# Optimization experiments

Hardware: AMD Instinct MI355X
Metric: run time of the kernel (lower is better)

The kernel has to match this reference:

```python
import jax, jax.numpy as jnp
import numpy as np

N = 25000
E = 400000
H = 8
C = 32
NEG_SLOPE = 0.2


def setup_inputs() -> dict:
    key = jax.random.key(0)
    ks = iter(jax.random.split(key, 64))
    d = {}
    d['x'] = jax.random.normal(next(ks), (N, 3), jnp.float32)
    d['edge_index'] = jax.random.randint(next(ks), (2, E), 0, N, dtype=jnp.int64)
    d['edge_attr'] = jax.random.uniform(next(ks), (E, 1), jnp.float32)
    # GATv2 layers: dims (in, concat): (3,T) -> (256,T) -> (256,F), out C=32, H=8
    dims = [(3, True), (H * C, True), (H * C, False)]
    for li, (din, concat) in enumerate(dims):
        d[f'Wl{li}'] = jax.random.normal(next(ks), (din, H * C), jnp.float32) * 0.05
        d[f'bl{li}'] = jnp.zeros((H * C,), jnp.float32)
        d[f'Wr{li}'] = jax.random.normal(next(ks), (din, H * C), jnp.float32) * 0.05
        d[f'br{li}'] = jnp.zeros((H * C,), jnp.float32)
        d[f'We{li}'] = jax.random.normal(next(ks), (1, H * C), jnp.float32) * 0.05
        d[f'att{li}'] = jax.random.normal(next(ks), (H, C), jnp.float32) * 0.05
        d[f'bias{li}'] = jnp.zeros((H * C if concat else C,), jnp.float32)
    # node head: Linear(32,32)-ReLU-Linear(32,2)
    d['nh_W1'] = jax.random.normal(next(ks), (C, C), jnp.float32) * 0.05
    d['nh_b1'] = jnp.zeros((C,), jnp.float32)
    d['nh_W2'] = jax.random.normal(next(ks), (C, 2), jnp.float32) * 0.05
    d['nh_b2'] = jnp.zeros((2,), jnp.float32)
    # edge head
    d['eh_W1'] = jax.random.normal(next(ks), (C, C), jnp.float32) * 0.05
    d['eh_b1'] = jnp.zeros((C,), jnp.float32)
    d['eh_W2'] = jax.random.normal(next(ks), (C, 2), jnp.float32) * 0.05
    d['eh_b2'] = jnp.zeros((2,), jnp.float32)
    return d


def _gatv2(x, src, dst, eattr, Wl, bl, Wr, br, We, att, bias, concat):
    n = x.shape[0]
    xl = (x @ Wl + bl).reshape(n, H, C)
    xr = (x @ Wr + br).reshape(n, H, C)
    em = (eattr @ We).reshape(-1, H, C)
    m = jax.nn.leaky_relu(xl[src] + xr[dst] + em, NEG_SLOPE)  # [Et,H,C]
    logit = jnp.einsum('ehc,hc->eh', m, att)                  # [Et,H]
    lmax = jax.ops.segment_max(logit, dst, num_segments=n)
    a = jnp.exp(logit - lmax[dst])
    alpha = a / jax.ops.segment_sum(a, dst, num_segments=n)[dst]
    out = jax.ops.segment_sum(xl[src] * alpha[..., None], dst, num_segments=n)
    out = out.reshape(n, H * C) if concat else out.mean(axis=1)
    return out + bias


def reference(x, edge_index, edge_attr,
              Wl0, bl0, Wr0, br0, We0, att0, bias0,
              Wl1, bl1, Wr1, br1, We1, att1, bias1,
              Wl2, bl2, Wr2, br2, We2, att2, bias2,
              nh_W1, nh_b1, nh_W2, nh_b2,
              eh_W1, eh_b1, eh_W2, eh_b2):
    src0, dst0 = edge_index[0], edge_index[1]
    n = x.shape[0]
    # add_self_loops with fill_value='mean' for edge_attr (PyG GATv2Conv default)
    deg = jax.ops.segment_sum(jnp.ones((src0.shape[0],), x.dtype), dst0, num_segments=n)
    loop_attr = jax.ops.segment_sum(edge_attr, dst0, num_segments=n) / jnp.maximum(deg, 1.0)[:, None]
    ar = jnp.arange(n, dtype=src0.dtype)
    src = jnp.concatenate([src0, ar])
    dst = jnp.concatenate([dst0, ar])
    eattr = jnp.concatenate([edge_attr, loop_attr], axis=0)

    layers = [
        (Wl0, bl0, Wr0, br0, We0, att0, bias0, True),
        (Wl1, bl1, Wr1, br1, We1, att1, bias1, True),
        (Wl2, bl2, Wr2, br2, We2, att2, bias2, False),
    ]
    h = x
    for (Wl, bl, Wr, br, We, att, bias, concat) in layers:
        h = _gatv2(h, src, dst, eattr, Wl, bl, Wr, br, We, att, bias, concat)
        h = jax.nn.relu(h)  # dropout is identity at eval

    node = jax.nn.log_softmax(jax.nn.relu(h @ nh_W1 + nh_b1) @ nh_W2 + nh_b2, axis=1)
    ef = h[src0] + h[dst0]
    edge = jax.nn.log_softmax(jax.nn.relu(ef @ eh_W1 + eh_b1) @ eh_W2 + eh_b2, axis=1)
    return node, edge
```

## Files before the change

kernel.cpp:

```cpp
#include <hip/hip_runtime.h>
#include <math.h>

#define HCDIM 256
#define HEADS 8
#define CH 32
#define NEG 0.2f
#define LOG2E 1.4426950408889634f

typedef __attribute__((ext_vector_type(8))) short bf16x8;
typedef __attribute__((ext_vector_type(4))) float f32x4;

__device__ __forceinline__ float4 ld4(const float* p){ return *reinterpret_cast<const float4*>(p); }
__device__ __forceinline__ void st4(float* p, float a, float b, float c, float d){
    float4 v; v.x=a; v.y=b; v.z=c; v.w=d; *reinterpret_cast<float4*>(p)=v;
}
__device__ __forceinline__ unsigned short f2bf(float f){
    union { float f; unsigned u; } x; x.f = f;
    unsigned r = x.u + 0x7fff + ((x.u >> 16) & 1);
    return (unsigned short)(r >> 16);
}
__device__ __forceinline__ float bf2f(unsigned short u){
    union { unsigned u; float f; } x; x.u = (unsigned)u << 16; return x.f;
}
__device__ __forceinline__ void unpk8(uint4 u, float* x){
    x[0] = __uint_as_float(u.x << 16); x[1] = __uint_as_float(u.x & 0xffff0000u);
    x[2] = __uint_as_float(u.y << 16); x[3] = __uint_as_float(u.y & 0xffff0000u);
    x[4] = __uint_as_float(u.z << 16); x[5] = __uint_as_float(u.z & 0xffff0000u);
    x[6] = __uint_as_float(u.w << 16); x[7] = __uint_as_float(u.w & 0xffff0000u);
}
__device__ __forceinline__ float dpp_sum4(float p){
    p += __int_as_float(__builtin_amdgcn_mov_dpp(__float_as_int(p), 0xB1, 0xf, 0xf, true));
    p += __int_as_float(__builtin_amdgcn_mov_dpp(__float_as_int(p), 0x4E, 0xf, 0xf, true));
    return p;
}

__global__ void k_count(const int* __restrict__ dst, const float* __restrict__ eattr,
                        unsigned long long* __restrict__ degsum,
                        int* __restrict__ rank, int E){
    int e = blockIdx.x*blockDim.x + threadIdx.x;
    if (e < E){
        int d = dst[e];
        unsigned long long pk = (1ULL << 40) |
            (unsigned long long)__float2uint_rn(eattr[e] * 1048576.0f);
        unsigned long long old = atomicAdd(&degsum[d], pk);
        rank[e] = (int)(old >> 40);
    }
}

__global__ __launch_bounds__(1024) void k_scan1(
        const unsigned long long* __restrict__ degsum,
        int* __restrict__ offs, float* __restrict__ lattr,
        int* __restrict__ partials, int n){
    __shared__ int wsum[16];
    int tid = threadIdx.x;
    int i = blockIdx.x*1024 + tid;
    int lane = tid & 63, wid = tid >> 6;
    int x = 0;
    if (i < n){
        unsigned long long ds = degsum[i];
        x = (int)(ds >> 40);
        float ls = (float)(ds & ((1ULL << 40) - 1)) * (1.0f/1048576.0f);
        lattr[i] = ls / fmaxf((float)x, 1.0f);
    }
    int v = x;
    #pragma unroll
    for (int o = 1; o < 64; o <<= 1){
        int y = __shfl_up(v, o);
        if (lane >= o) v += y;
    }
    if (lane == 63) wsum[wid] = v;
    __syncthreads();
    if (wid == 0 && lane < 16){
        int w = wsum[lane];
        #pragma unroll
        for (int o = 1; o < 16; o <<= 1){
            int y = __shfl_up(w, o);
            if (lane >= o) w += y;
        }
        wsum[lane] = w;
    }
    __syncthreads();
    int incl = v + (wid > 0 ? wsum[wid-1] : 0);
    if (i < n) offs[i+1] = incl;
    if (tid == 1023) partials[blockIdx.x] = incl;
}

__global__ __launch_bounds__(1024) void k_scan3(int* __restrict__ offs,
                                                const int* __restrict__ partials, int n){
    __shared__ int sbase;
    if (threadIdx.x < 64){
        int lane = threadIdx.x;
        int vv = (lane < (int)blockIdx.x) ? partials[lane] : 0;
        #pragma unroll
        for (int o = 1; o < 64; o <<= 1) vv += __shfl_xor(vv, o);
        if (lane == 0) sbase = vv;
    }
    __syncthreads();
    int i = blockIdx.x*1024 + threadIdx.x;
    if (i < n) offs[i+1] += sbase;
    if (i == 0) offs[0] = 0;
}

__global__ void k_scatter(const int* __restrict__ src, const int* __restrict__ dst,
                          const float* __restrict__ eattr, const int* __restrict__ offs,
                          const int* __restrict__ rank, int2* csr, int E){
    int e = blockIdx.x*blockDim.x + threadIdx.x;
    if (e < E){
        int d = dst[e];
        int pos = offs[d] + rank[e];
        int2 pk; pk.x = src[e] << 9; pk.y = __float_as_int(eattr[e]);
        csr[pos] = pk;
    }
}

__global__ __launch_bounds__(256) void k_dualgemm(
        const float* __restrict__ h, int din,
        const float* __restrict__ Wl, const float* __restrict__ bl,
        const float* __restrict__ Wr, const float* __restrict__ br,
        unsigned short* __restrict__ xl, unsigned short* __restrict__ xr, int n)
{
    const int ROWS = 16;
    __shared__ float hs[ROWS * HCDIM];
    int row0 = blockIdx.x * ROWS;
    int j = threadIdx.x;

    for (int idx = threadIdx.x; idx < ROWS*din; idx += 256){
        int r = idx / din, k = idx - r*din;
        int row = row0 + r;
        hs[r*din + k] = (row < n) ? h[(size_t)row*din + k] : 0.f;
    }
    __syncthreads();

    float accl[ROWS], accr[ROWS];
    float blj = bl[j], brj = br[j];
    #pragma unroll
    for (int r = 0; r < ROWS; r++){ accl[r] = blj; accr[r] = brj; }

    for (int k = 0; k < din; k++){
        float wl = Wl[k*HCDIM + j], wr = Wr[k*HCDIM + j];
        #pragma unroll
        for (int r = 0; r < ROWS; r++){
            float hv = hs[r*din + k];
            accl[r] += hv*wl;
            accr[r] += hv*wr;
        }
    }
    #pragma unroll
    for (int r = 0; r < ROWS; r++){
        int row = row0 + r;
        if (row < n){
            xl[(size_t)row*HCDIM + j] = f2bf(accl[r]);
            xr[(size_t)row*HCDIM + j] = f2bf(accr[r]);
        }
    }
}

__global__ __launch_bounds__(256) void k_cvtw2(
        const float* __restrict__ Wl1, const float* __restrict__ Wr1,
        const float* __restrict__ Wl2, const float* __restrict__ Wr2,
        unsigned short* __restrict__ Wt1, unsigned short* __restrict__ Wt2)
{
    int idx = blockIdx.x*256 + threadIdx.x;
    int half = idx >> 17;
    int j = idx & 131071;
    int nout = j >> 8, k = j & 255;
    const float* Wl = half ? Wl2 : Wl1;
    const float* Wr = half ? Wr2 : Wr1;
    float v = (nout < 256) ? Wl[k*HCDIM + nout] : Wr[k*HCDIM + (nout - 256)];
    (half ? Wt2 : Wt1)[j] = f2bf(v);
}

#define BM 128
#define BN 128
#define BK 32
#define LDK 40

__global__ __launch_bounds__(256) void k_mfma_gemm(
        const unsigned short* __restrict__ h,
        const unsigned short* __restrict__ Wt,
        const float* __restrict__ bl, const float* __restrict__ br,
        unsigned short* __restrict__ xl, unsigned short* __restrict__ xr, int n)
{
    __shared__ unsigned short As[BM*LDK];
    __shared__ unsigned short Bs[BN*LDK];
    int tid = threadIdx.x;
    int row0 = blockIdx.x * BM;
    int col0 = blockIdx.y * BN;

    int l = tid & 63, w = tid >> 6;
    int wm = (w >> 1) * 64, wn = (w & 1) * 64;

    f32x4 acc[4][4] = {};

    int srow = tid >> 1;
    int skoff = (tid & 1) * 16;

    for (int kt = 0; kt < 8; ++kt){
        int kb = kt * BK;
        uint4 av0, av1;
        int grow = row0 + srow;
        if (grow < n){
            const uint4* ap = reinterpret_cast<const uint4*>(h + (size_t)grow*HCDIM + kb + skoff);
            av0 = ap[0]; av1 = ap[1];
        } else {
            av0.x=av0.y=av0.z=av0.w=0u; av1 = av0;
        }
        const uint4* bp = reinterpret_cast<const uint4*>(Wt + (size_t)(col0+srow)*HCDIM + kb + skoff);
        uint4 bv0 = bp[0], bv1 = bp[1];

        __syncthreads();

        *reinterpret_cast<uint4*>(&As[srow*LDK + skoff])     = av0;
        *reinterpret_cast<uint4*>(&As[srow*LDK + skoff + 8]) = av1;
        *reinterpret_cast<uint4*>(&Bs[srow*LDK + skoff])     = bv0;
        *reinterpret_cast<uint4*>(&Bs[srow*LDK + skoff + 8]) = bv1;

        __syncthreads();

        bf16x8 af[4], bfr[4];
        #pragma unroll
        for (int m = 0; m < 4; m++)
            af[m] = *reinterpret_cast<const bf16x8*>(&As[(wm + m*16 + (l & 15))*LDK + ((l >> 4)*8)]);
        #pragma unroll
        for (int nn = 0; nn < 4; nn++)
            bfr[nn] = *reinterpret_cast<const bf16x8*>(&Bs[(wn + nn*16 + (l & 15))*LDK + ((l >> 4)*8)]);
        #pragma unroll
        for (int m = 0; m < 4; m++)
            #pragma unroll
            for (int nn = 0; nn < 4; nn++)
                acc[m][nn] = __builtin_amdgcn_mfma_f32_16x16x32_bf16(af[m], bfr[nn], acc[m][nn], 0, 0, 0);
    }

    unsigned short* dstp; const float* biasp; int cbase;
    if (col0 < 256){ dstp = xl; biasp = bl; cbase = col0; }
    else           { dstp = xr; biasp = br; cbase = col0 - 256; }

    #pragma unroll
    for (int nn = 0; nn < 4; nn++){
        int gc = cbase + wn + nn*16 + (l & 15);
        float bb = biasp[gc];
        #pragma unroll
        for (int m = 0; m < 4; m++){
            int r0 = row0 + wm + m*16 + ((l >> 4) * 4);
            #pragma unroll
            for (int v = 0; v < 4; v++){
                int rr = r0 + v;
                if (rr < n) dstp[(size_t)rr*HCDIM + gc] = f2bf(acc[m][nn][v] + bb);
            }
        }
    }
}

__global__ __launch_bounds__(256) void k_gat(
        const unsigned short* __restrict__ xl, const unsigned short* __restrict__ xr,
        const int2* __restrict__ csr,
        const int* __restrict__ offs, const float* __restrict__ lattr,
        const float* __restrict__ We, const float* __restrict__ att,
        const float* __restrict__ bias,
        unsigned short* __restrict__ hout_bf, float* __restrict__ hout_f,
        int n, int concat)
{
    int wid  = threadIdx.x >> 6;
    int lane = threadIdx.x & 63;
    int v = blockIdx.x*4 + wid;
    if (v >= n) return;
    int sub = lane >> 5;
    int l5  = lane & 31;
    const char* xlb = reinterpret_cast<const char*>(xl);
    const size_t cbb = (size_t)l5 * 16;

    float We8[8], at8[8], xr8[8];
    {
        const float* wp = We + l5*8;
        const float* ap = att + l5*8;
        #pragma unroll
        for (int c = 0; c < 8; c++){ We8[c] = wp[c]; at8[c] = ap[c]*LOG2E; }
        uint4 u = *reinterpret_cast<const uint4*>(xr + (size_t)v*HCDIM + l5*8);
        unpk8(u, xr8);
    }
    int pbeg = offs[v], pend = offs[v+1];
    float la = lattr[v];

    float s = 0.f;
    float acc[8] = {0.f,0.f,0.f,0.f,0.f,0.f,0.f,0.f};

    auto estep = [&](uint4 xu, float ea){
        float x8[8];
        unpk8(xu, x8);
        float part = 0.f;
        #pragma unroll
        for (int c = 0; c < 8; c++){
            float t = x8[c] + fmaf(ea, We8[c], xr8[c]);
            t = fmaxf(t, NEG*t);
            part = fmaf(t, at8[c], part);
        }
        part = dpp_sum4(part);
        float w = __builtin_amdgcn_exp2f(part);
        s += w;
        #pragma unroll
        for (int c = 0; c < 8; c++) acc[c] = fmaf(w, x8[c], acc[c]);
    };

    {
        uint4 xu; float ea; bool act;
        if (sub == 0){
            xu = *reinterpret_cast<const uint4*>(xlb + ((size_t)v << 9) + cbb);
            ea = la; act = true;
        } else {
            act = (pbeg < pend);
            if (act){
                int2 e = csr[pbeg];
                xu = *reinterpret_cast<const uint4*>(xlb + (size_t)(unsigned)e.x + cbb);
                ea = __int_as_float(e.y);
            }
        }
        if (act) estep(xu, ea);
    }

    int p = pbeg + 1;
    int2 e; uint4 xup; bool act = false;
    {
        int idx = p + sub;
        act = (idx < pend);
        if (act){
            e = csr[idx];
            xup = *reinterpret_cast<const uint4*>(xlb + (size_t)(unsigned)e.x + cbb);
        }
    }
    for (; p < pend; p += 2){
        uint4 cx = xup; float cea = __int_as_float(e.y); bool cact = act;
        int nidx = p + 2 + sub;
        act = (nidx < pend);
        if (act){
            e = csr[nidx];
            xup = *reinterpret_cast<const uint4*>(xlb + (size_t)(unsigned)e.x + cbb);
        }
        if (cact) estep(cx, cea);
    }

    s += __shfl_xor(s, 32);
    #pragma unroll
    for (int c = 0; c < 8; c++) acc[c] += __shfl_xor(acc[c], 32);

    float inv = 1.f / s;
    if (concat){
        if (sub == 0){
            const float* bp = bias + l5*8;
            float4 b0 = ld4(bp), b1 = ld4(bp + 4);
            float r0 = fmaxf(fmaf(acc[0], inv, b0.x), 0.f);
            float r1 = fmaxf(fmaf(acc[1], inv, b0.y), 0.f);
            float r2 = fmaxf(fmaf(acc[2], inv, b0.z), 0.f);
            float r3 = fmaxf(fmaf(acc[3], inv, b0.w), 0.f);
            float r4 = fmaxf(fmaf(acc[4], inv, b1.x), 0.f);
            float r5 = fmaxf(fmaf(acc[5], inv, b1.y), 0.f);
            float r6 = fmaxf(fmaf(acc[6], inv, b1.z), 0.f);
            float r7 = fmaxf(fmaf(acc[7], inv, b1.w), 0.f);
            uint4 o;
            o.x = (unsigned)f2bf(r0) | ((unsigned)f2bf(r1) << 16);
            o.y = (unsigned)f2bf(r2) | ((unsigned)f2bf(r3) << 16);
            o.z = (unsigned)f2bf(r4) | ((unsigned)f2bf(r5) << 16);
            o.w = (unsigned)f2bf(r6) | ((unsigned)f2bf(r7) << 16);
            *reinterpret_cast<uint4*>(hout_bf + (size_t)v*HCDIM + l5*8) = o;
        }
    } else {
        float o8[8];
        #pragma unroll
        for (int c = 0; c < 8; c++) o8[c] = acc[c]*inv;
        #pragma unroll
        for (int m = 4; m <= 16; m <<= 1)
            #pragma unroll
            for (int c = 0; c < 8; c++) o8[c] += __shfl_xor(o8[c], m);
        if (lane < 4){
            const float* bp = bias + lane*8;
            float4 b0 = ld4(bp), b1 = ld4(bp + 4);
            float* op = hout_f + (size_t)v*CH + lane*8;
            st4(op,   fmaxf(fmaf(o8[0], 0.125f, b0.x), 0.f),
                      fmaxf(fmaf(o8[1], 0.125f, b0.y), 0.f),
                      fmaxf(fmaf(o8[2], 0.125f, b0.z), 0.f),
                      fmaxf(fmaf(o8[3], 0.125f, b0.w), 0.f));
            st4(op+4, fmaxf(fmaf(o8[4], 0.125f, b1.x), 0.f),
                      fmaxf(fmaf(o8[5], 0.125f, b1.y), 0.f),
                      fmaxf(fmaf(o8[6], 0.125f, b1.z), 0.f),
                      fmaxf(fmaf(o8[7], 0.125f, b1.w), 0.f));
        }
    }
}

__global__ __launch_bounds__(256) void k_heads(
        const float* __restrict__ hf,
        const float* __restrict__ nW1, const float* __restrict__ nb1,
        const float* __restrict__ nW2, const float* __restrict__ nb2,
        const float* __restrict__ eW1,
        float* __restrict__ out, unsigned short* __restrict__ Pe, int count)
{
    __shared__ float sh[8][CH];
    int g = threadIdx.x >> 5;
    int t = threadIdx.x & 31;
    int i = blockIdx.x*8 + g;
    sh[g][t] = (i < count) ? hf[(size_t)i*CH + t] : 0.f;
    __syncthreads();
    float z = nb1[t];
    float pe = 0.f;
    #pragma unroll
    for (int k = 0; k < CH; k++){
        float hk = sh[g][k];
        z  = fmaf(hk, nW1[k*CH + t], z);
        pe = fmaf(hk, eW1[k*CH + t], pe);
    }
    if (i < count) Pe[(size_t)i*CH + t] = f2bf(pe);
    z = fmaxf(z, 0.f);
    float r0 = z * nW2[t*2 + 0];
    float r1 = z * nW2[t*2 + 1];
    #pragma unroll
    for (int o = 1; o < 32; o <<= 1){
        r0 += __shfl_xor(r0, o);
        r1 += __shfl_xor(r1, o);
    }
    if (t == 0 && i < count){
        float z0 = r0 + nb2[0], z1 = r1 + nb2[1];
        float mm = fmaxf(z0, z1);
        float lse = mm + __logf(__expf(z0 - mm) + __expf(z1 - mm));
        out[(size_t)i*2 + 0] = z0 - lse;
        out[(size_t)i*2 + 1] = z1 - lse;
    }
}

__global__ __launch_bounds__(256) void k_edgefin(
        const unsigned short* __restrict__ P,
        const int* __restrict__ src, const int* __restrict__ dst,
        const float* __restrict__ b1, const float* __restrict__ W2,
        const float* __restrict__ b2, float* __restrict__ out, int E)
{
    int gt = blockIdx.x*256 + threadIdx.x;
    int e = gt >> 3, sub = gt & 7;
    if (e >= E) return;
    int s = src[e], d = dst[e];
    int c0 = sub*4;
    ushort4 us = *reinterpret_cast<const ushort4*>(P + (size_t)s*CH + c0);
    ushort4 ud = *reinterpret_cast<const ushort4*>(P + (size_t)d*CH + c0);
    float4 bb = ld4(b1 + c0);
    float zx = fmaxf(bf2f(us.x) + bf2f(ud.x) + bb.x, 0.f);
    float zy = fmaxf(bf2f(us.y) + bf2f(ud.y) + bb.y, 0.f);
    float zz = fmaxf(bf2f(us.z) + bf2f(ud.z) + bb.z, 0.f);
    float zw = fmaxf(bf2f(us.w) + bf2f(ud.w) + bb.w, 0.f);
    float r0 = zx*W2[(c0+0)*2] + zy*W2[(c0+1)*2] + zz*W2[(c0+2)*2] + zw*W2[(c0+3)*2];
    float r1 = zx*W2[(c0+0)*2+1] + zy*W2[(c0+1)*2+1] + zz*W2[(c0+2)*2+1] + zw*W2[(c0+3)*2+1];
    #pragma unroll
    for (int o = 1; o < 8; o <<= 1){
        r0 += __shfl_xor(r0, o);
        r1 += __shfl_xor(r1, o);
    }
    if (sub == 0){
        float z0 = r0 + b2[0], z1 = r1 + b2[1];
        float mm = fmaxf(z0, z1);
        float lse = mm + __logf(__expf(z0 - mm) + __expf(z1 - mm));
        float2 o2; o2.x = z0 - lse; o2.y = z1 - lse;
        *reinterpret_cast<float2*>(out + (size_t)e*2) = o2;
    }
}

extern "C" void kernel_launch(void* const* d_in, const int* in_sizes, int n_in,
                              void* d_out, int out_size, void* d_ws, size_t ws_size,
                              hipStream_t stream)
{
    const float* x     = (const float*)d_in[0];
    const int*   ei    = (const int*)d_in[1];
    const float* eattr = (const float*)d_in[2];
    int N = in_sizes[0] / 3;
    int E = in_sizes[2];
    const int* src0 = ei;
    const int* dst0 = ei + E;

    const float *Wl[3], *bl[3], *Wr[3], *br[3], *We[3], *att[3], *bias[3];
    for (int l = 0; l < 3; l++){
        int b = 3 + l*7;
        Wl[l]   = (const float*)d_in[b+0];
        bl[l]   = (const float*)d_in[b+1];
        Wr[l]   = (const float*)d_in[b+2];
        br[l]   = (const float*)d_in[b+3];
        We[l]   = (const float*)d_in[b+4];
        att[l]  = (const float*)d_in[b+5];
        bias[l] = (const float*)d_in[b+6];
    }
    const float* nhW1 = (const float*)d_in[24];
    const float* nhb1 = (const float*)d_in[25];
    const float* nhW2 = (const float*)d_in[26];
    const float* nhb2 = (const float*)d_in[27];
    const float* ehW1 = (const float*)d_in[28];
    const float* ehb1 = (const float*)d_in[29];
    const float* ehW2 = (const float*)d_in[30];
    const float* ehb2 = (const float*)d_in[31];

    char* ws = (char*)d_ws;
    auto alloc = [&](size_t bytes) -> char* {
        char* p = ws;
        ws += (bytes + 255) & ~(size_t)255;
        return p;
    };
    unsigned short* Hb  = (unsigned short*)alloc((size_t)N*HCDIM*2);
    float* H0f          = (float*)alloc((size_t)N*CH*4);
    unsigned short* XL  = (unsigned short*)alloc((size_t)N*HCDIM*2);
    unsigned short* XR  = (unsigned short*)alloc((size_t)N*HCDIM*2);
    unsigned long long* degsum = (unsigned long long*)alloc((size_t)N*8);
    int*   rank     = (int*)alloc((size_t)E*4);
    float* lattr    = (float*)alloc((size_t)N*4);
    int*   offs     = (int*)alloc((size_t)(N+1)*4);
    int*   partials = (int*)alloc((size_t)64*4);
    int2*  csr      = (int2*)alloc((size_t)E*8);
    unsigned short* Wt1 = (unsigned short*)alloc((size_t)512*HCDIM*2);
    unsigned short* Wt2 = (unsigned short*)alloc((size_t)512*HCDIM*2);
    unsigned short* Pe  = (unsigned short*)alloc((size_t)N*CH*2);

    int nb = (N + 1023) / 1024;

    (void)hipMemsetAsync(degsum, 0, (size_t)N*8, stream);
    k_count<<<(E+255)/256, 256, 0, stream>>>(dst0, eattr, degsum, rank, E);
    k_scan1<<<nb, 1024, 0, stream>>>(degsum, offs, lattr, partials, N);
    k_scan3<<<nb, 1024, 0, stream>>>(offs, partials, N);
    k_scatter<<<(E+255)/256, 256, 0, stream>>>(src0, dst0, eattr, offs, rank, csr, E);
    k_cvtw2<<<1024, 256, 0, stream>>>(Wl[1], Wr[1], Wl[2], Wr[2], Wt1, Wt2);

    int gat_grid  = (N + 3) / 4;
    dim3 mfma_grid((N + BM - 1) / BM, 4);

    k_dualgemm<<<(N+15)/16, 256, 0, stream>>>(x, 3, Wl[0], bl[0], Wr[0], br[0], XL, XR, N);
    k_gat<<<gat_grid, 256, 0, stream>>>(XL, XR, csr, offs, lattr,
                                        We[0], att[0], bias[0], Hb, nullptr, N, 1);
    k_mfma_gemm<<<mfma_grid, 256, 0, stream>>>(Hb, Wt1, bl[1], br[1], XL, XR, N);
    k_gat<<<gat_grid, 256, 0, stream>>>(XL, XR, csr, offs, lattr,
                                        We[1], att[1], bias[1], Hb, nullptr, N, 1);
    k_mfma_gemm<<<mfma_grid, 256, 0, stream>>>(Hb, Wt2, bl[2], br[2], XL, XR, N);
    k_gat<<<gat_grid, 256, 0, stream>>>(XL, XR, csr, offs, lattr,
                                        We[2], att[2], bias[2], nullptr, H0f, N, 0);

    float* out_node = (float*)d_out;
    float* out_edge = out_node + (size_t)N*2;
    k_heads<<<(N+7)/8, 256, 0, stream>>>(H0f, nhW1, nhb1, nhW2, nhb2, ehW1,
                                         out_node, Pe, N);
    k_edgefin<<<((size_t)E*8 + 255)/256, 256, 0, stream>>>(Pe, src0, dst0,
                                                           ehb1, ehW2, ehb2, out_edge, E);
}
```

Measured before the change: 261.7 us.

## Fuse preprocessing kernels, add XCD-aware GEMM block remap, widen edge head per thread

Merges the degree-count, first-layer dual GEMM (specialised for 3 input features) and weight bf16 conversion into one launch that picks its role by block index, removing two kernel launches. Remaps the MFMA GEMM to a 1D grid whose blocks are reordered so that consecutive logical tiles land on the same XCD, aiming for better L2 reuse of A rows. The edge-head kernel now has each thread process 8 channels with 16-byte loads and reduces across 4 lanes with DPP instead of 8-lane shuffles, halving thread count. The fused kernel mixes heterogeneous block roles, which may leave some blocks imbalanced.

Result: faster. 254.6 us (-2.7%).

```diff
diff --git a/kernel.cpp b/kernel.cpp
--- a/kernel.cpp
+++ b/kernel.cpp
@@ -34,16 +34,63 @@
     return p;
 }
 
-__global__ void k_count(const int* __restrict__ dst, const float* __restrict__ eattr,
-                        unsigned long long* __restrict__ degsum,
-                        int* __restrict__ rank, int E){
-    int e = blockIdx.x*blockDim.x + threadIdx.x;
-    if (e < E){
-        int d = dst[e];
-        unsigned long long pk = (1ULL << 40) |
-            (unsigned long long)__float2uint_rn(eattr[e] * 1048576.0f);
-        unsigned long long old = atomicAdd(&degsum[d], pk);
-        rank[e] = (int)(old >> 40);
+__global__ __launch_bounds__(256) void k_fused_pre(
+        const int* __restrict__ dst, const float* __restrict__ eattr,
+        unsigned long long* __restrict__ degsum, int* __restrict__ rank, int E,
+        const float* __restrict__ x,
+        const float* __restrict__ Wl0, const float* __restrict__ bl0,
+        const float* __restrict__ Wr0, const float* __restrict__ br0,
+        unsigned short* __restrict__ XL, unsigned short* __restrict__ XR, int N,
+        const float* __restrict__ Wl1, const float* __restrict__ Wr1,
+        const float* __restrict__ Wl2, const float* __restrict__ Wr2,
+        unsigned short* __restrict__ Wt1, unsigned short* __restrict__ Wt2,
+        int nbCount, int nbGemm)
+{
+    __shared__ float hs[48];
+    int b = blockIdx.x;
+    int tid = threadIdx.x;
+    if (b < nbCount){
+        int e = b*256 + tid;
+        if (e < E){
+            int d = dst[e];
+            unsigned long long pk = (1ULL << 40) |
+                (unsigned long long)__float2uint_rn(eattr[e] * 1048576.0f);
+            unsigned long long old = atomicAdd(&degsum[d], pk);
+            rank[e] = (int)(old >> 40);
+        }
+    } else if (b < nbCount + nbGemm){
+        int gb = b - nbCount;
+        int row0 = gb * 16;
+        if (tid < 48){
+            int r = tid / 3, c = tid - r*3;
+            int row = row0 + r;
+            hs[tid] = (row < N) ? x[(size_t)row*3 + c] : 0.f;
+        }
+        __syncthreads();
+        int j = tid;
+        float wl0 = Wl0[j], wl1 = Wl0[256 + j], wl2 = Wl0[512 + j];
+        float wr0 = Wr0[j], wr1 = Wr0[256 + j], wr2 = Wr0[512 + j];
+        float blj = bl0[j], brj = br0[j];
+        #pragma unroll
+        for (int r = 0; r < 16; r++){
+            int row = row0 + r;
+            if (row < N){
+                float h0 = hs[r*3], h1 = hs[r*3+1], h2 = hs[r*3+2];
+                float al = blj + h0*wl0 + h1*wl1 + h2*wl2;
+                float ar = brj + h0*wr0 + h1*wr1 + h2*wr2;
+                XL[(size_t)row*HCDIM + j] = f2bf(al);
+                XR[(size_t)row*HCDIM + j] = f2bf(ar);
+            }
+        }
+    } else {
+        int idx = (b - nbCount - nbGemm)*256 + tid;
+        int half = idx >> 17;
+        int j = idx & 131071;
+        int nout = j >> 8, k = j & 255;
+        const float* Wl = half ? Wl2 : Wl1;
+        const float* Wr = half ? Wr2 : Wr1;
+        float v = (nout < 256) ? Wl[k*HCDIM + nout] : Wr[k*HCDIM + (nout - 256)];
+        (half ? Wt2 : Wt1)[j] = f2bf(v);
     }
 }
 
@@ -113,63 +160,6 @@
     }
 }
 
-__global__ __launch_bounds__(256) void k_dualgemm(
-        const float* __restrict__ h, int din,
-        const float* __restrict__ Wl, const float* __restrict__ bl,
-        const float* __restrict__ Wr, const float* __restrict__ br,
-        unsigned short* __restrict__ xl, unsigned short* __restrict__ xr, int n)
-{
-    const int ROWS = 16;
-    __shared__ float hs[ROWS * HCDIM];
-    int row0 = blockIdx.x * ROWS;
-    int j = threadIdx.x;
-
-    for (int idx = threadIdx.x; idx < ROWS*din; idx += 256){
-        int r = idx / din, k = idx - r*din;
-        int row = row0 + r;
-        hs[r*din + k] = (row < n) ? h[(size_t)row*din + k] : 0.f;
-    }
-    __syncthreads();
-
-    float accl[ROWS], accr[ROWS];
-    float blj = bl[j], brj = br[j];
-    #pragma unroll
-    for (int r = 0; r < ROWS; r++){ accl[r] = blj; accr[r] = brj; }
-
-    for (int k = 0; k < din; k++){
-        float wl = Wl[k*HCDIM + j], wr = Wr[k*HCDIM + j];
-        #pragma unroll
-        for (int r = 0; r < ROWS; r++){
-            float hv = hs[r*din + k];
-            accl[r] += hv*wl;
-            accr[r] += hv*wr;
-        }
-    }
-    #pragma unroll
-    for (int r = 0; r < ROWS; r++){
-        int row = row0 + r;
-        if (row < n){
-            xl[(size_t)row*HCDIM + j] = f2bf(accl[r]);
-            xr[(size_t)row*HCDIM + j] = f2bf(accr[r]);
-        }
-    }
-}
-
-__global__ __launch_bounds__(256) void k_cvtw2(
-        const float* __restrict__ Wl1, const float* __restrict__ Wr1,
-        const float* __restrict__ Wl2, const float* __restrict__ Wr2,
-        unsigned short* __restrict__ Wt1, unsigned short* __restrict__ Wt2)
-{
-    int idx = blockIdx.x*256 + threadIdx.x;
-    int half = idx >> 17;
-    int j = idx & 131071;
-    int nout = j >> 8, k = j & 255;
-    const float* Wl = half ? Wl2 : Wl1;
-    const float* Wr = half ? Wr2 : Wr1;
-    float v = (nout < 256) ? Wl[k*HCDIM + nout] : Wr[k*HCDIM + (nout - 256)];
-    (half ? Wt2 : Wt1)[j] = f2bf(v);
-}
-
 #define BM 128
 #define BN 128
 #define BK 32
@@ -184,8 +174,12 @@
     __shared__ unsigned short As[BM*LDK];
     __shared__ unsigned short Bs[BN*LDK];
     int tid = threadIdx.x;
-    int row0 = blockIdx.x * BM;
-    int col0 = blockIdx.y * BN;
+    int total = gridDim.x;
+    int q = total >> 3, rr = total & 7;
+    int xcd = blockIdx.x & 7, slot = blockIdx.x >> 3;
+    int logical = (xcd < rr ? xcd*(q+1) : rr*(q+1) + (xcd-rr)*q) + slot;
+    int row0 = (logical >> 2) * BM;
+    int col0 = (logical & 3) * BN;
 
     int l = tid & 63, w = tid >> 6;
     int wm = (w >> 1) * 64, wn = (w & 1) * 64;
@@ -244,8 +238,8 @@
             int r0 = row0 + wm + m*16 + ((l >> 4) * 4);
             #pragma unroll
             for (int v = 0; v < 4; v++){
-                int rr = r0 + v;
-                if (rr < n) dstp[(size_t)rr*HCDIM + gc] = f2bf(acc[m][nn][v] + bb);
+                int rr2 = r0 + v;
+                if (rr2 < n) dstp[(size_t)rr2*HCDIM + gc] = f2bf(acc[m][nn][v] + bb);
             }
         }
     }
@@ -432,24 +426,26 @@
         const float* __restrict__ b2, float* __restrict__ out, int E)
 {
     int gt = blockIdx.x*256 + threadIdx.x;
-    int e = gt >> 3, sub = gt & 7;
+    int e = gt >> 2, sub = gt & 3;
     if (e >= E) return;
     int s = src[e], d = dst[e];
-    int c0 = sub*4;
-    ushort4 us = *reinterpret_cast<const ushort4*>(P + (size_t)s*CH + c0);
-    ushort4 ud = *reinterpret_cast<const ushort4*>(P + (size_t)d*CH + c0);
-    float4 bb = ld4(b1 + c0);
-    float zx = fmaxf(bf2f(us.x) + bf2f(ud.x) + bb.x, 0.f);
-    float zy = fmaxf(bf2f(us.y) + bf2f(ud.y) + bb.y, 0.f);
-    float zz = fmaxf(bf2f(us.z) + bf2f(ud.z) + bb.z, 0.f);
-    float zw = fmaxf(bf2f(us.w) + bf2f(ud.w) + bb.w, 0.f);
-    float r0 = zx*W2[(c0+0)*2] + zy*W2[(c0+1)*2] + zz*W2[(c0+2)*2] + zw*W2[(c0+3)*2];
-    float r1 = zx*W2[(c0+0)*2+1] + zy*W2[(c0+1)*2+1] + zz*W2[(c0+2)*2+1] + zw*W2[(c0+3)*2+1];
+    int c0 = sub*8;
+    uint4 us = *reinterpret_cast<const uint4*>(P + (size_t)s*CH + c0);
+    uint4 ud = *reinterpret_cast<const uint4*>(P + (size_t)d*CH + c0);
+    float ps[8], pd[8];
+    unpk8(us, ps); unpk8(ud, pd);
+    const float* bp = b1 + c0;
+    float4 bb0 = ld4(bp), bb1 = ld4(bp + 4);
+    float b8[8] = {bb0.x, bb0.y, bb0.z, bb0.w, bb1.x, bb1.y, bb1.z, bb1.w};
+    float r0 = 0.f, r1 = 0.f;
     #pragma unroll
-    for (int o = 1; o < 8; o <<= 1){
-        r0 += __shfl_xor(r0, o);
-        r1 += __shfl_xor(r1, o);
-    }
+    for (int c = 0; c < 8; c++){
+        float z = fmaxf(ps[c] + pd[c] + b8[c], 0.f);
+        r0 = fmaf(z, W2[(c0+c)*2 + 0], r0);
+        r1 = fmaf(z, W2[(c0+c)*2 + 1], r1);
+    }
+    r0 = dpp_sum4(r0);
+    r1 = dpp_sum4(r1);
     if (sub == 0){
         float z0 = r0 + b2[0], z1 = r1 + b2[1];
         float mm = fmaxf(z0, z1);
@@ -512,24 +508,29 @@
     unsigned short* Pe  = (unsigned short*)alloc((size_t)N*CH*2);
 
     int nb = (N + 1023) / 1024;
+    int nbCount = (E + 255) / 256;
+    int nbGemm  = (N + 15) / 16;
+    int nbCvt   = 1024;
 
     (void)hipMemsetAsync(degsum, 0, (size_t)N*8, stream);
-    k_count<<<(E+255)/256, 256, 0, stream>>>(dst0, eattr, degsum, rank, E);
+    k_fused_pre<<<nbCount + nbGemm + nbCvt, 256, 0, stream>>>(
+        dst0, eattr, degsum, rank, E,
+        x, Wl[0], bl[0], Wr[0], br[0], XL, XR, N,
+        Wl[1], Wr[1], Wl[2], Wr[2], Wt1, Wt2,
+        nbCount, nbGemm);
     k_scan1<<<nb, 1024, 0, stream>>>(degsum, offs, lattr, partials, N);
     k_scan3<<<nb, 1024, 0, stream>>>(offs, partials, N);
     k_scatter<<<(E+255)/256, 256, 0, stream>>>(src0, dst0, eattr, offs, rank, csr, E);
-    k_cvtw2<<<1024, 256, 0, stream>>>(Wl[1], Wr[1], Wl[2], Wr[2], Wt1, Wt2);
 
     int gat_grid  = (N + 3) / 4;
-    dim3 mfma_grid((N + BM - 1) / BM, 4);
-
-    k_dualgemm<<<(N+15)/16, 256, 0, stream>>>(x, 3, Wl[0], bl[0], Wr[0], br[0], XL, XR, N);
+    int gemm_grid = ((N + BM - 1) / BM) * 4;
+
     k_gat<<<gat_grid, 256, 0, stream>>>(XL, XR, csr, offs, lattr,
                                         We[0], att[0], bias[0], Hb, nullptr, N, 1);
-    k_mfma_gemm<<<mfma_grid, 256, 0, stream>>>(Hb, Wt1, bl[1], br[1], XL, XR, N);
+    k_mfma_gemm<<<gemm_grid, 256, 0, stream>>>(Hb, Wt1, bl[1], br[1], XL, XR, N);
     k_gat<<<gat_grid, 256, 0, stream>>>(XL, XR, csr, offs, lattr,
                                         We[1], att[1], bias[1], Hb, nullptr, N, 1);
-    k_mfma_gemm<<<mfma_grid, 256, 0, stream>>>(Hb, Wt2, bl[2], br[2], XL, XR, N);
+    k_mfma_gemm<<<gemm_grid, 256, 0, stream>>>(Hb, Wt2, bl[2], br[2], XL, XR, N);
     k_gat<<<gat_grid, 256, 0, stream>>>(XL, XR, csr, offs, lattr,
                                         We[2], att[2], bias[2], nullptr, H0f, N, 0);
 
@@ -537,6 +538,6 @@
     float* out_edge = out_node + (size_t)N*2;
     k_heads<<<(N+7)/8, 256, 0, stream>>>(H0f, nhW1, nhb1, nhW2, nhb2, ehW1,
                                          out_node, Pe, N);
-    k_edgefin<<<((size_t)E*8 + 255)/256, 256, 0, stream>>>(Pe, src0, dst0,
+    k_edgefin<<<((size_t)E*4 + 255)/256, 256, 0, stream>>>(Pe, src0, dst0,
                                                            ehb1, ehW2, ehb2, out_edge, E);
 }
```
